# Kernel optimization log

Measured on AMD Instinct MI355X. Metric: run time of the kernel, lower is better.

Reference implementation:

```python
import jax, jax.numpy as jnp
import numpy as np

B, Hh, Ww, C = 8, 64, 64, 384
Dg = C // 2          # 192, per-group d_model
Di = Dg              # expand=1 -> d_inner = d_model
K = 2                # scan directions per group
S = 1                # d_state
R = -(-Dg // 16)     # dt_rank = ceil(d_model/16) = 12
Cout = 384


def setup_inputs() -> dict:
    key = jax.random.key(0)
    ks = jax.random.split(key, 30)
    n = lambda k, shp, s=0.05: (jax.random.normal(k, shp, jnp.float32) * s)
    inp = {
        "x": jax.random.normal(ks[0], (B, Hh * Ww, C), jnp.float32),
        "norm_g": jnp.ones((C,), jnp.float32),
        "norm_b": jnp.zeros((C,), jnp.float32),
        # DynamicChannelSorter (reduction=2)
        "r_w1": n(ks[1], (C // 2, C)), "r_b1": n(ks[2], (C // 2,)),
        "r_w2": n(ks[3], (C, C // 2)), "r_b2": n(ks[4], (C,)),
        # SS2D params stacked over 2 groups
        "in_proj_w": n(ks[5], (2, 2 * Di, Dg)),
        "conv_w": n(ks[6], (2, Di, 1, 3, 3), 0.1),
        "conv_b": n(ks[7], (2, Di), 0.02),
        "x_proj_w": n(ks[8], (2, K, R + 2 * S, Di)),
        "dt_proj_w": n(ks[9], (2, K, Di, R), 0.1),
        "dt_proj_b": n(ks[10], (2, K, Di), 0.5) - 3.0,   # softplus-inv of small dt
        "A_log": n(ks[11], (2, K, Di, S), 0.1),
        "Ds": jnp.ones((2, K, Di), jnp.float32),
        "out_norm_g": jnp.ones((2, Di), jnp.float32),
        "out_norm_b": jnp.zeros((2, Di), jnp.float32),
        "out_proj_w": n(ks[12], (2, Dg, Di)),
        # channel_interaction (reduction=16)
        "ci_w1": n(ks[13], (C // 16, C)), "ci_b1": n(ks[14], (C // 16,)),
        "ci_w2": n(ks[15], (C, C // 16)), "ci_b2": n(ks[16], (C,)),
        "proj_w": n(ks[17], (Cout, C)), "proj_b": n(ks[18], (Cout,)),
        "skip_scale": jnp.ones((1,), jnp.float32),
        "H": Hh, "W": Ww,
    }
    return inp


def _ln(x, g, b, eps=1e-5):
    m = x.mean(-1, keepdims=True)
    v = jnp.mean((x - m) ** 2, -1, keepdims=True)
    return (x - m) * jax.lax.rsqrt(v + eps) * g + b


def _selective_scan(xs, dts, Bm, Cm, A, D):
    # xs,dts: (B,K,Di,L); Bm,Cm: (B,K,S,L); A: (K,Di,S); D: (K,Di)
    dA = jnp.exp(dts[..., None] * A[None, :, :, None, :])              # (B,K,Di,L,S)
    dBx = dts[..., None] * jnp.swapaxes(Bm, -1, -2)[:, :, None] * xs[..., None]
    dA_t = jnp.moveaxis(dA, 3, 0)                                      # (L,B,K,Di,S)
    dBx_t = jnp.moveaxis(dBx, 3, 0)
    C_t = jnp.moveaxis(Cm, -1, 0)                                      # (L,B,K,S)
    h0 = jnp.zeros(dA.shape[:3] + (dA.shape[-1],), xs.dtype)           # (B,K,Di,S)

    def step(h, inp):
        a, bx, c = inp
        h = a * h + bx
        return h, jnp.einsum('bkcs,bks->bkc', h, c)

    _, ys = jax.lax.scan(step, h0, (dA_t, dBx_t, C_t))                 # (L,B,K,Di)
    ys = jnp.moveaxis(ys, 0, -1)                                       # (B,K,Di,L)
    return ys + D[None, :, :, None] * xs


def _ss2d(x, in_w, cw, cb, xp_w, dt_w, dt_b, A_log, D, on_g, on_b, op_w, vertical):
    # x: (B,H,W,Dg). VMamba-style SS2D with K=2 directions.
    b, h, w, _ = x.shape
    L = h * w
    xz = jnp.einsum('bhwc,dc->bhwd', x, in_w)                          # (B,H,W,2*Di)
    xc, z = jnp.split(xz, 2, axis=-1)
    xc = jnp.transpose(xc, (0, 3, 1, 2))                               # (B,Di,H,W)
    xc = jax.lax.conv_general_dilated(
        xc, cw, (1, 1), 'SAME', feature_group_count=Di,
        dimension_numbers=('NCHW', 'OIHW', 'NCHW')) + cb[None, :, None, None]
    xc = jax.nn.silu(xc)
    xf = jnp.transpose(xc, (0, 1, 3, 2)) if vertical else xc
    xflat = xf.reshape(b, Di, L)
    xs = jnp.stack([xflat, jnp.flip(xflat, -1)], axis=1)               # (B,K,Di,L)
    x_dbl = jnp.einsum('bkcl,kdc->bkdl', xs, xp_w)
    r = dt_w.shape[-1]
    dts, Bm, Cm = x_dbl[:, :, :r], x_dbl[:, :, r:r + S], x_dbl[:, :, r + S:r + 2 * S]
    dts = jax.nn.softplus(jnp.einsum('bkrl,kdr->bkdl', dts, dt_w) + dt_b[None, :, :, None])
    A = -jnp.exp(A_log)
    ys = _selective_scan(xs, dts, Bm, Cm, A, D)                        # (B,K,Di,L)
    y = ys[:, 0] + jnp.flip(ys[:, 1], -1)                              # cross-merge
    if vertical:
        y = jnp.transpose(y.reshape(b, Di, w, h), (0, 1, 3, 2))
    else:
        y = y.reshape(b, Di, h, w)
    y = jnp.transpose(y, (0, 2, 3, 1))                                 # (B,H,W,Di)
    y = _ln(y, on_g, on_b)
    y = y * jax.nn.silu(z)
    return jnp.einsum('bhwd,od->bhwo', y, op_w)


def reference(x, norm_g, norm_b, r_w1, r_b1, r_w2, r_b2, in_proj_w, conv_w,
              conv_b, x_proj_w, dt_proj_w, dt_proj_b, A_log, Ds, out_norm_g,
              out_norm_b, out_proj_w, ci_w1, ci_b1, ci_w2, ci_b2, proj_w,
              proj_b, skip_scale, H, W):
    b, n, c = x.shape
    residual = x
    xn = _ln(x, norm_g, norm_b)
    # dynamic channel sorter
    pool = xn.mean(axis=1)                                             # (B,C)
    scores = jax.nn.sigmoid(jax.nn.relu(pool @ r_w1.T + r_b1) @ r_w2.T + r_b2)
    sort_idx = jnp.argsort(-scores, axis=1)
    inv_idx = jnp.argsort(sort_idx, axis=1)
    x_sorted = jnp.take_along_axis(xn, sort_idx[:, None, :], axis=2)
    xsp = x_sorted.reshape(b, H, W, c)
    x1, x2 = jnp.split(xsp, 2, axis=-1)
    y1 = _ss2d(x1, in_proj_w[0], conv_w[0], conv_b[0], x_proj_w[0], dt_proj_w[0],
               dt_proj_b[0], A_log[0], Ds[0], out_norm_g[0], out_norm_b[0],
               out_proj_w[0], vertical=False)
    y2 = _ss2d(x2, in_proj_w[1], conv_w[1], conv_b[1], x_proj_w[1], dt_proj_w[1],
               dt_proj_b[1], A_log[1], Ds[1], out_norm_g[1], out_norm_b[1],
               out_proj_w[1], vertical=True)
    y_cat = jnp.concatenate([y1, y2], axis=-1).reshape(b, n, c)
    y_restored = jnp.take_along_axis(y_cat, inv_idx[:, None, :], axis=2)
    gate = jax.nn.sigmoid(jax.nn.relu(xn @ ci_w1.T + ci_b1) @ ci_w2.T + ci_b2)
    y_final = (y_restored * gate) @ proj_w.T + proj_b
    return residual + y_final * skip_scale
```

## Files before the change

kernel.cpp:

```cpp
#include <hip/hip_runtime.h>
#include <math.h>

#define NB 8
#define LTOK 4096
#define CH 384
#define DH 192
#define HH 64
#define WW 64
#define NCHK 128
#define CHS 32

static constexpr long BLC  = (long)NB * LTOK * CH;
static constexpr long CST  = (long)32 * NCHK * DH;

typedef unsigned short u16;
typedef u16   u16x8 __attribute__((ext_vector_type(8)));
typedef short s16x8 __attribute__((ext_vector_type(8)));
typedef float f32x4 __attribute__((ext_vector_type(4)));

__device__ inline u16 f2bf(float f){
  unsigned int u = __float_as_uint(f);
  return (u16)((u + 0x7FFFu + ((u >> 16) & 1u)) >> 16);
}
__device__ inline float bf2f(u16 h){ return __uint_as_float(((unsigned int)h) << 16); }
__device__ inline float fsigmoid(float x){ return 1.f / (1.f + __expf(-x)); }

#define SCOL(ml, c) ((c) ^ ((((ml) >> 2) & 3) << 4))

template<int NW>
__device__ inline float blockSum(float v, float* sm){
  #pragma unroll
  for (int o = 32; o > 0; o >>= 1) v += __shfl_down(v, o);
  int lane = threadIdx.x & 63, wv = threadIdx.x >> 6;
  if (lane == 0) sm[wv] = v;
  __syncthreads();
  if (threadIdx.x == 0){ float t = 0.f; for (int i = 0; i < NW; i++) t += sm[i]; sm[0] = t; }
  __syncthreads();
  float t = sm[0];
  __syncthreads();
  return t;
}

__global__ __launch_bounds__(128) void k_ln(const float* __restrict__ x,
    const float* __restrict__ g, const float* __restrict__ b, float* __restrict__ xn){
  __shared__ float sm[2];
  long row = blockIdx.x;
  int t = threadIdx.x;
  const float* xr = x + row * CH;
  float v0 = xr[t], v1 = xr[t + 128], v2 = xr[t + 256];
  float s = blockSum<2>(v0 + v1 + v2, sm);
  float m = s * (1.f / CH);
  float d0 = v0 - m, d1 = v1 - m, d2 = v2 - m;
  float vs = blockSum<2>(d0*d0 + d1*d1 + d2*d2, sm);
  float inv = rsqrtf(vs * (1.f / CH) + 1e-5f);
  float* o = xn + row * CH;
  o[t]       = d0 * inv * g[t]       + b[t];
  o[t + 128] = d1 * inv * g[t + 128] + b[t + 128];
  o[t + 256] = d2 * inv * g[t + 256] + b[t + 256];
}

__global__ __launch_bounds__(128) void k_pool(const float* __restrict__ xn, float* __restrict__ pp){
  int c = blockIdx.x * 128 + threadIdx.x;
  int chunk = blockIdx.y, b = blockIdx.z;
  long base = ((long)b * LTOK + chunk * 256) * CH;
  float s = 0.f;
  for (int n = 0; n < 256; n++) s += xn[base + (long)n * CH + c];
  pp[((long)b * 16 + chunk) * CH + c] = s;
}

__global__ __launch_bounds__(384) void k_score(const float* __restrict__ pp,
    const float* __restrict__ w1, const float* __restrict__ b1,
    const float* __restrict__ w2, const float* __restrict__ b2,
    int* __restrict__ sidx, int* __restrict__ inv){
  __shared__ float poolv[CH];
  __shared__ float hid[192];
  __shared__ float sc[CH];
  int b = blockIdx.x, t = threadIdx.x;
  float s = 0.f;
  for (int ch = 0; ch < 16; ch++) s += pp[((long)b * 16 + ch) * CH + t];
  poolv[t] = s * (1.f / LTOK);
  __syncthreads();
  if (t < 192){
    float h = b1[t];
    for (int c = 0; c < CH; c++) h += poolv[c] * w1[t * CH + c];
    hid[t] = fmaxf(h, 0.f);
  }
  __syncthreads();
  {
    float h = b2[t];
    for (int j = 0; j < 192; j++) h += hid[j] * w2[t * 192 + j];
    sc[t] = 1.f / (1.f + expf(-h));
  }
  __syncthreads();
  float mys = sc[t];
  int rank = 0;
  for (int j = 0; j < CH; j++){
    float o = sc[j];
    rank += (o > mys) || (o == mys && j < t);
  }
  sidx[b * CH + rank] = t;
  inv[b * CH + t] = rank;
}

__global__ __launch_bounds__(256) void k_cast(const float* __restrict__ s,
    u16* __restrict__ d, int n){
  int i = blockIdx.x * 256 + threadIdx.x;
  if (i < n) d[i] = f2bf(s[i]);
}

__global__ __launch_bounds__(256) void k_prepA(const float* __restrict__ alog,
    float* __restrict__ Atab){
  int i = blockIdx.x * 256 + threadIdx.x;
  if (i < 4 * 192) Atab[i] = -expf(alog[i]);
}

__global__ __launch_bounds__(256) void k_prepcw(const float* __restrict__ cw,
    u16* __restrict__ cwb){
  int i = blockIdx.x * 256 + threadIdx.x;
  if (i < 2 * 9 * DH){
    int g = i / (9 * DH); int r = i - g * 9 * DH;
    int tap = r / DH; int di = r - tap * DH;
    cwb[i] = f2bf(cw[((long)g * DH + di) * 9 + tap]);
  }
}

__global__ __launch_bounds__(384) void k_castgather(const float* __restrict__ xn,
    const int* __restrict__ sidx, u16* __restrict__ As){
  long row = blockIdx.x;
  int b = (int)(row >> 12);
  int t = threadIdx.x;
  int c = sidx[b * CH + t];
  As[row * CH + t] = f2bf(xn[row * CH + c]);
}

__global__ __launch_bounds__(256) void k_prepw(const float* __restrict__ w1,
    const float* __restrict__ b1, const float* __restrict__ w2,
    const int* __restrict__ sidx, u16* __restrict__ w1g, u16* __restrict__ w2p,
    float* __restrict__ b1p){
  int b = blockIdx.x, tid = threadIdx.x;
  if (b < NB){
    const int* sx = sidx + b * CH;
    for (int i = tid; i < 32 * CH; i += 256){
      int j = i / CH, r = i - j * CH;
      float v = (j < 24) ? w1[j * CH + sx[r]] : 0.f;
      w1g[(long)b * 32 * CH + i] = f2bf(v);
    }
  } else {
    for (int i = tid; i < CH * 32; i += 256){
      int n = i >> 5, j = i & 31;
      w2p[i] = f2bf((j < 24) ? w2[n * 24 + j] : 0.f);
    }
    if (tid < 32) b1p[tid] = (tid < 24) ? b1[tid] : 0.f;
  }
}

__global__ __launch_bounds__(256) void k_prepM(const float* __restrict__ dtw,
    const float* __restrict__ xpw, u16* __restrict__ Mw){
  int gk = blockIdx.y;
  int g = gk >> 1, k = gk & 1;
  int idx = blockIdx.x * 256 + threadIdx.x;
  int di = idx / 192, c = idx - di * 192;
  float s = 0.f;
  #pragma unroll
  for (int r = 0; r < 12; r++)
    s += dtw[((long)gk * 192 + di) * 12 + r] * xpw[(long)g * 5376 + (k * 14 + r) * 192 + c];
  Mw[(long)gk * 36864 + idx] = f2bf(s);
}

__global__ __launch_bounds__(256) void k_hid(const u16* __restrict__ As,
    const u16* __restrict__ w1g, const float* __restrict__ b1p,
    u16* __restrict__ hidp){
  __shared__ u16 sA[128 * 32];
  __shared__ u16 sB[32 * 32];
  int b = blockIdx.y;
  const u16* Ab = As + (long)b * LTOK * CH;
  const u16* Bb = w1g + (long)b * 32 * CH;
  int tid = threadIdx.x;
  int m0 = blockIdx.x * 128;
  int wv = tid >> 6, l = tid & 63;
  int wm = wv * 32;
  int kg = l >> 4, lr = l & 15;

  f32x4 acc[2][2];
  #pragma unroll
  for (int i = 0; i < 2; i++)
    #pragma unroll
    for (int j = 0; j < 2; j++)
      #pragma unroll
      for (int r = 0; r < 4; r++) acc[i][j][r] = 0.f;

  int aoffU[2], boffU[2];
  #pragma unroll
  for (int i = 0; i < 2; i++){
    int r = wm + i * 16 + lr;
    aoffU[i] = r * 32 + ((kg * 8) ^ ((r & 3) << 3));
  }
  #pragma unroll
  for (int j = 0; j < 2; j++){
    int r = j * 16 + lr;
    boffU[j] = r * 32 + ((kg * 8) ^ ((r & 3) << 3));
  }

  u16x8 ra[2], rbv;
  #pragma unroll
  for (int q = 0; q < 2; q++){
    int i = q * 256 + tid; int row = i >> 2, sl = i & 3, ss = sl ^ (row & 3);
    ra[q] = *(const u16x8*)(Ab + (long)(m0 + row) * CH + ss * 8);
  }
  if (tid < 128){
    int row = tid >> 2, sl = tid & 3, ss = sl ^ (row & 3);
    rbv = *(const u16x8*)(Bb + (long)row * CH + ss * 8);
  }

  const int nks = CH / 32;
  for (int ks = 0; ks < nks; ks++){
    __syncthreads();
    #pragma unroll
    for (int q = 0; q < 2; q++){
      int i = q * 256 + tid; int row = i >> 2, sl = i & 3;
      *(u16x8*)(sA + row * 32 + sl * 8) = ra[q];
    }
    if (tid < 128){
      int row = tid >> 2, sl = tid & 3;
      *(u16x8*)(sB + row * 32 + sl * 8) = rbv;
    }
    __syncthreads();
    if (ks + 1 < nks){
      int k0 = (ks + 1) * 32;
      #pragma unroll
      for (int q = 0; q < 2; q++){
        int i = q * 256 + tid; int row = i >> 2, sl = i & 3, ss = sl ^ (row & 3);
        ra[q] = *(const u16x8*)(Ab + (long)(m0 + row) * CH + k0 + ss * 8);
      }
      if (tid < 128){
        int row = tid >> 2, sl = tid & 3, ss = sl ^ (row & 3);
        rbv = *(const u16x8*)(Bb + (long)row * CH + k0 + ss * 8);
      }
    }
    s16x8 af[2], bfr[2];
    #pragma unroll
    for (int i = 0; i < 2; i++) af[i] = *(const s16x8*)(sA + aoffU[i]);
    #pragma unroll
    for (int j = 0; j < 2; j++) bfr[j] = *(const s16x8*)(sB + boffU[j]);
    #pragma unroll
    for (int i = 0; i < 2; i++)
      #pragma unroll
      for (int j = 0; j < 2; j++)
        acc[i][j] = __builtin_amdgcn_mfma_f32_16x16x32_bf16(af[i], bfr[j], acc[i][j], 0, 0, 0);
  }

  #pragma unroll
  for (int i = 0; i < 2; i++)
    #pragma unroll
    for (int j = 0; j < 2; j++)
      #pragma unroll
      for (int r = 0; r < 4; r++){
        int m = m0 + wm + i * 16 + kg * 4 + r;
        int n = j * 16 + lr;
        float v = fmaxf(acc[i][j][r] + b1p[n], 0.f);
        hidp[((long)b * LTOK + m) * 32 + n] = f2bf(v);
      }
}

template<int BN, int MODE>
__global__ __launch_bounds__(256) void k_mm(
    const u16* __restrict__ A, int lda, long aOuter, long aInner,
    const u16* __restrict__ B, long bInner,
    float* __restrict__ Cf, u16* __restrict__ Ch,
    long cOuter, long cInner, int ldc,
    int K, int innerCnt,
    const float* __restrict__ bias, const float* __restrict__ resid,
    const float* __restrict__ skip,
    const u16* __restrict__ gy, const int* __restrict__ ginv){
  constexpr int BM = 128;
  constexpr int AI = 2;
  constexpr int BI = (BN * 32) / (256 * 8);
  constexpr int NJ = BN / 32;
  __shared__ u16 sA[BM * 32];
  __shared__ u16 sB[BN * 32];

  int bz = blockIdx.z;
  int bo = bz / innerCnt, bi_ = bz - bo * innerCnt;
  const u16* Ab = A + (long)bo * aOuter + (long)bi_ * aInner;
  const u16* Bb = B + (long)bi_ * bInner;
  int tid = threadIdx.x;
  int m0 = blockIdx.y * BM, n0 = blockIdx.x * BN;
  int wv = tid >> 6, l = tid & 63;
  int wm = (wv >> 1) * 64, wn = (wv & 1) * (BN / 2);
  int kg = l >> 4, lr = l & 15;

  f32x4 acc[4][NJ];
  #pragma unroll
  for (int i = 0; i < 4; i++)
    #pragma unroll
    for (int j = 0; j < NJ; j++)
      #pragma unroll
      for (int r = 0; r < 4; r++) acc[i][j][r] = 0.f;

  int aoffU[4], boffU[NJ];
  #pragma unroll
  for (int i = 0; i < 4; i++){
    int r = wm + i * 16 + lr;
    aoffU[i] = r * 32 + ((kg * 8) ^ ((r & 3) << 3));
  }
  #pragma unroll
  for (int j = 0; j < NJ; j++){
    int r = wn + j * 16 + lr;
    boffU[j] = r * 32 + ((kg * 8) ^ ((r & 3) << 3));
  }

  u16x8 ra[AI], rb[BI];
  #pragma unroll
  for (int q = 0; q < AI; q++){
    int i = q * 256 + tid; int row = i >> 2, sl = i & 3, ss = sl ^ (row & 3);
    ra[q] = *(const u16x8*)(Ab + (long)(m0 + row) * lda + ss * 8);
  }
  #pragma unroll
  for (int q = 0; q < BI; q++){
    int i = q * 256 + tid; int row = i >> 2, sl = i & 3, ss = sl ^ (row & 3);
    rb[q] = *(const u16x8*)(Bb + (long)(n0 + row) * K + ss * 8);
  }

  int nks = K >> 5;
  for (int ks = 0; ks < nks; ks++){
    __syncthreads();
    #pragma unroll
    for (int q = 0; q < AI; q++){
      int i = q * 256 + tid; int row = i >> 2, sl = i & 3;
      *(u16x8*)(sA + row * 32 + sl * 8) = ra[q];
    }
    #pragma unroll
    for (int q = 0; q < BI; q++){
      int i = q * 256 + tid; int row = i >> 2, sl = i & 3;
      *(u16x8*)(sB + row * 32 + sl * 8) = rb[q];
    }
    __syncthreads();
    if (ks + 1 < nks){
      int k0 = (ks + 1) * 32;
      #pragma unroll
      for (int q = 0; q < AI; q++){
        int i = q * 256 + tid; int row = i >> 2, sl = i & 3, ss = sl ^ (row & 3);
        ra[q] = *(const u16x8*)(Ab + (long)(m0 + row) * lda + k0 + ss * 8);
      }
      #pragma unroll
      for (int q = 0; q < BI; q++){
        int i = q * 256 + tid; int row = i >> 2, sl = i & 3, ss = sl ^ (row & 3);
        rb[q] = *(const u16x8*)(Bb + (long)(n0 + row) * K + k0 + ss * 8);
      }
    }
    s16x8 af[4];
    #pragma unroll
    for (int i = 0; i < 4; i++) af[i] = *(const s16x8*)(sA + aoffU[i]);
    s16x8 bfr[NJ];
    #pragma unroll
    for (int j = 0; j < NJ; j++) bfr[j] = *(const s16x8*)(sB + boffU[j]);
    #pragma unroll
    for (int i = 0; i < 4; i++)
      #pragma unroll
      for (int j = 0; j < NJ; j++)
        acc[i][j] = __builtin_amdgcn_mfma_f32_16x16x32_bf16(af[i], bfr[j], acc[i][j], 0, 0, 0);
  }

  long zc = (long)bo * cOuter + (long)bi_ * cInner;
  #pragma unroll
  for (int i = 0; i < 4; i++){
    #pragma unroll
    for (int j = 0; j < NJ; j++){
      #pragma unroll
      for (int r = 0; r < 4; r++){
        int m = m0 + wm + i * 16 + kg * 4 + r;
        int n = n0 + wn + j * 16 + lr;
        float v = acc[i][j][r];
        if constexpr (MODE == 1){
          if (n < 192) ((u16*)Cf)[zc + (long)m * 192 + n] = f2bf(v);
          else         Ch[zc + (long)m * 192 + (n - 192)] = f2bf(v);
        } else if constexpr (MODE == 2){
          Ch[zc + (long)m * ldc + n] = f2bf(v);
        } else if constexpr (MODE == 3){
          float vb = v + bias[n];
          long o = (long)m * ldc + n;
          Cf[o] = resid[o] + skip[0] * vb;
        } else {
          float gate = fsigmoid(v + bias[n]);
          int bt = m >> 12;
          float yr = bf2f(gy[(long)m * ldc + ginv[bt * CH + n]]);
          Ch[(long)m * ldc + n] = f2bf(yr * gate);
        }
      }
    }
  }
}

__global__ __launch_bounds__(256) void k_dt(
    const u16* __restrict__ xcvh, const u16* __restrict__ Mw,
    const float* __restrict__ dtb, const float* __restrict__ Atab,
    const float* __restrict__ bc, u16* __restrict__ pk16,
    float* __restrict__ cP, float* __restrict__ cS){
  constexpr int BM = 128, AI = 2, NJ = 2;
  __shared__ unsigned sMem[BM * 64];
  u16* sA  = (u16*)sMem;
  u16* sB  = (u16*)(sMem + 2048);
  u16* xvT = (u16*)(sMem + 3072);

  int z = blockIdx.z;
  int bg = z >> 1, kk_ = z & 1, g = bg & 1, gk = g * 2 + kk_;
  const u16* Ab = xcvh + (long)bg * LTOK * 192;
  const u16* Bb = Mw + (long)gk * 36864;
  int tid = threadIdx.x;
  int m0 = blockIdx.y * BM, n0 = blockIdx.x * 64;
  int wv = tid >> 6, l = tid & 63;
  int wm = (wv >> 1) * 64, wn = (wv & 1) * 32;
  int kg = l >> 4, lr = l & 15;

  #pragma unroll
  for (int q = 0; q < 4; q++){
    int i8 = q * 256 + tid;
    int row = i8 >> 3, c8 = i8 & 7;
    u16x8 v = *(const u16x8*)(Ab + (long)(m0 + row) * 192 + n0 + c8 * 8);
    *(u16x8*)(xvT + row * 72 + c8 * 8) = v;
  }

  f32x4 acc[4][NJ];
  #pragma unroll
  for (int i = 0; i < 4; i++)
    #pragma unroll
    for (int j = 0; j < NJ; j++)
      #pragma unroll
      for (int r = 0; r < 4; r++) acc[i][j][r] = 0.f;

  int aoffU[4], boffU[NJ];
  #pragma unroll
  for (int i = 0; i < 4; i++){
    int r = wm + i * 16 + lr;
    aoffU[i] = r * 32 + ((kg * 8) ^ ((r & 3) << 3));
  }
  #pragma unroll
  for (int j = 0; j < NJ; j++){
    int r = wn + j * 16 + lr;
    boffU[j] = r * 32 + ((kg * 8) ^ ((r & 3) << 3));
  }

  u16x8 ra[AI], rb0;
  #pragma unroll
  for (int q = 0; q < AI; q++){
    int i = q * 256 + tid; int row = i >> 2, sl = i & 3, ss = sl ^ (row & 3);
    ra[q] = *(const u16x8*)(Ab + (long)(m0 + row) * 192 + ss * 8);
  }
  {
    int row = tid >> 2, sl = tid & 3, ss = sl ^ (row & 3);
    rb0 = *(const u16x8*)(Bb + (long)(n0 + row) * 192 + ss * 8);
  }

  const int nks = 6;
  for (int ks = 0; ks < nks; ks++){
    __syncthreads();
    #pragma unroll
    for (int q = 0; q < AI; q++){
      int i = q * 256 + tid; int row = i >> 2, sl = i & 3;
      *(u16x8*)(sA + row * 32 + sl * 8) = ra[q];
    }
    {
      int row = tid >> 2, sl = tid & 3;
      *(u16x8*)(sB + row * 32 + sl * 8) = rb0;
    }
    __syncthreads();
    if (ks + 1 < nks){
      int k0 = (ks + 1) * 32;
      #pragma unroll
      for (int q = 0; q < AI; q++){
        int i = q * 256 + tid; int row = i >> 2, sl = i & 3, ss = sl ^ (row & 3);
        ra[q] = *(const u16x8*)(Ab + (long)(m0 + row) * 192 + k0 + ss * 8);
      }
      {
        int row = tid >> 2, sl = tid & 3, ss = sl ^ (row & 3);
        rb0 = *(const u16x8*)(Bb + (long)(n0 + row) * 192 + k0 + ss * 8);
      }
    }
    s16x8 af[4], bfr[NJ];
    #pragma unroll
    for (int i = 0; i < 4; i++) af[i] = *(const s16x8*)(sA + aoffU[i]);
    #pragma unroll
    for (int j = 0; j < NJ; j++) bfr[j] = *(const s16x8*)(sB + boffU[j]);
    #pragma unroll
    for (int i = 0; i < 4; i++)
      #pragma unroll
      for (int j = 0; j < NJ; j++)
        acc[i][j] = __builtin_amdgcn_mfma_f32_16x16x32_bf16(af[i], bfr[j], acc[i][j], 0, 0, 0);
  }

  unsigned pkreg[4][NJ][4];
  float dtbj[NJ], Atlj[NJ];
  #pragma unroll
  for (int j = 0; j < NJ; j++){
    int n = n0 + wn + j * 16 + lr;
    dtbj[j] = dtb[gk * 192 + n];
    Atlj[j] = Atab[gk * 192 + n];
  }
  #pragma unroll
  for (int i = 0; i < 4; i++){
    #pragma unroll
    for (int r = 0; r < 4; r++){
      int ml = wm + i * 16 + kg * 4 + r;
      int m = m0 + ml;
      float Bv = bc[((long)z * LTOK + m) * 2];
      #pragma unroll
      for (int j = 0; j < NJ; j++){
        int n = n0 + wn + j * 16 + lr;
        float rr = acc[i][j][r] + dtbj[j];
        float dtv = __logf(1.f + __expf(rr));
        float av  = __expf(Atlj[j] * dtv);
        float xv  = bf2f(xvT[ml * 72 + wn + j * 16 + lr]);
        pk16[((long)z * LTOK + m) * 192 + n] = f2bf(dtv);
        pkreg[i][j][r] = ((unsigned)f2bf(dtv * Bv * xv) << 16) | (unsigned)f2bf(av);
      }
    }
  }

  __syncthreads();
  #pragma unroll
  for (int i = 0; i < 4; i++){
    #pragma unroll
    for (int j = 0; j < NJ; j++){
      #pragma unroll
      for (int r = 0; r < 4; r++){
        int ml = wm + i * 16 + kg * 4 + r;
        int cl = wn + j * 16 + lr;
        sMem[ml * 64 + SCOL(ml, cl)] = pkreg[i][j][r];
      }
    }
  }
  __syncthreads();

  int cc = tid >> 6, nn = tid & 63;
  float P = 1.f, S = 0.f;
  if (kk_ == 0){
    for (int s = 0; s < CHS; s++){
      int row = cc * CHS + s;
      unsigned v = sMem[row * 64 + SCOL(row, nn)];
      float a = bf2f((u16)(v & 0xFFFFu));
      float dBx = bf2f((u16)(v >> 16));
      P *= a; S = a * S + dBx;
    }
  } else {
    for (int s = CHS - 1; s >= 0; s--){
      int row = cc * CHS + s;
      unsigned v = sMem[row * 64 + SCOL(row, nn)];
      float a = bf2f((u16)(v & 0xFFFFu));
      float dBx = bf2f((u16)(v >> 16));
      P *= a; S = a * S + dBx;
    }
  }
  int cglob = (kk_ == 0) ? (blockIdx.y * 4 + cc)
                         : ((LTOK - m0) / CHS - cc - 1);
  long idx = ((long)z * NCHK + cglob) * 192 + n0 + nn;
  cP[idx] = P;
  cS[idx] = S;
}

__global__ __launch_bounds__(192) void k_conv(const u16* __restrict__ xch,
    const u16* __restrict__ cwb, const float* __restrict__ cb,
    const float* __restrict__ xpw, u16* __restrict__ xcvh,
    float* __restrict__ bc){
  __shared__ float red[8][4][25];
  int tid = threadIdx.x;
  int chg = tid % 24, pp = tid / 24;
  int p = blockIdx.x * 8 + pp;
  int bg = blockIdx.y; int g = bg & 1;
  int h = p >> 6, w = p & 63;
  int di = chg * 8;
  long sb = (long)bg * LTOK;

  u16x8 wv[9];
  #pragma unroll
  for (int t = 0; t < 9; t++)
    wv[t] = *(const u16x8*)(cwb + ((long)g * 9 + t) * DH + di);

  float acc[8];
  #pragma unroll
  for (int j = 0; j < 8; j++) acc[j] = cb[g * DH + di + j];

  #pragma unroll
  for (int dh = -1; dh <= 1; dh++){
    int hh = h + dh; if (hh < 0 || hh >= HH) continue;
    #pragma unroll
    for (int dw = -1; dw <= 1; dw++){
      int ww2 = w + dw; if (ww2 < 0 || ww2 >= WW) continue;
      u16x8 xv = *(const u16x8*)(xch + (sb + hh * WW + ww2) * DH + di);
      int t = (dh + 1) * 3 + (dw + 1);
      #pragma unroll
      for (int j = 0; j < 8; j++) acc[j] += bf2f(wv[t][j]) * bf2f(xv[j]);
    }
  }

  u16x8 ov;
  #pragma unroll
  for (int j = 0; j < 8; j++){
    float s = acc[j];
    acc[j] = s * fsigmoid(s);
    ov[j] = f2bf(acc[j]);
  }
  int lscan = (g == 0) ? p : (w * HH + h);
  *(u16x8*)(xcvh + (sb + lscan) * DH + di) = ov;

  #pragma unroll
  for (int j = 0; j < 4; j++){
    int k = j >> 1, ci = j & 1;
    const float* wl = xpw + (long)g * 5376 + (k * 14 + 12 + ci) * 192 + di;
    float sacc = 0.f;
    #pragma unroll
    for (int q = 0; q < 8; q++) sacc += acc[q] * wl[q];
    red[pp][j][chg] = sacc;
  }
  __syncthreads();
  if (tid < 32){
    int pos = tid >> 2, j = tid & 3;
    float ssum = 0.f;
    #pragma unroll
    for (int q = 0; q < 24; q++) ssum += red[pos][j][q];
    int p2 = blockIdx.x * 8 + pos;
    int h2 = p2 >> 6, w2 = p2 & 63;
    int ls = (g == 0) ? p2 : (w2 * HH + h2);
    int k = j >> 1;
    bc[(((long)(bg * 2 + k)) * LTOK + ls) * 2 + (j & 1)] = ssum;
  }
}

__global__ __launch_bounds__(192) void k_scan_p2(const float* __restrict__ cP,
    const float* __restrict__ cS, float* __restrict__ h0){
  int z = blockIdx.x;
  int di = threadIdx.x;
  float h = 0.f;
  for (int c = 0; c < NCHK; c++){
    long idx = ((long)z * NCHK + c) * 192 + di;
    h0[idx] = h;
    h = cP[idx] * h + cS[idx];
  }
}

__global__ __launch_bounds__(192) void k_scan_p3(const u16* __restrict__ pk16,
    const u16* __restrict__ xcvh, const float* __restrict__ bc,
    const float* __restrict__ Atab, const float* __restrict__ ds,
    const float* __restrict__ h0, const u16* __restrict__ zh,
    const float* __restrict__ ong, const float* __restrict__ onb,
    u16* __restrict__ yab){
  __shared__ float yl[CHS][193];
  __shared__ float red[2][32][6];
  __shared__ float minv[2][32];
  int bg = blockIdx.x, c = blockIdx.y;
  int g = bg & 1;
  int di = threadIdx.x;
  const u16* xc = xcvh + (long)bg * LTOK * 192 + di;
  int l0 = c * CHS;
  float yv[CHS];

  {
    int z = bg * 2, gk = g * 2;
    float Dv = ds[gk * 192 + di], Av = Atab[gk * 192 + di];
    const u16* pk = pk16 + (long)z * LTOK * 192 + di;
    const float* bcp = bc + (long)z * LTOK * 2;
    float h = h0[((long)z * NCHK + c) * 192 + di];
    #pragma unroll
    for (int s = 0; s < CHS; s++){
      int l = l0 + s;
      float dtv = bf2f(pk[(long)l * 192]);
      float av  = __expf(Av * dtv);
      float xv  = bf2f(xc[(long)l * 192]);
      float Bv  = bcp[l * 2], Cv = bcp[l * 2 + 1];
      h = av * h + dtv * Bv * xv;
      yv[s] = h * Cv + Dv * xv;
    }
  }
  {
    int z = bg * 2 + 1, gk = g * 2 + 1;
    float Dv = ds[gk * 192 + di], Av = Atab[gk * 192 + di];
    const u16* pk = pk16 + (long)z * LTOK * 192 + di;
    const float* bcp = bc + (long)z * LTOK * 2;
    int cc = NCHK - 1 - c;
    float h = h0[((long)z * NCHK + cc) * 192 + di];
    #pragma unroll
    for (int s = CHS - 1; s >= 0; s--){
      int l = l0 + s;
      float dtv = bf2f(pk[(long)l * 192]);
      float av  = __expf(Av * dtv);
      float xv  = bf2f(xc[(long)l * 192]);
      float Bv  = bcp[l * 2], Cv = bcp[l * 2 + 1];
      h = av * h + dtv * Bv * xv;
      yv[s] += h * Cv + Dv * xv;
    }
  }

  #pragma unroll
  for (int s = 0; s < CHS; s++) yl[s][di] = yv[s];
  __syncthreads();
  {
    int pos = di & 31, seg = di >> 5;
    float s1 = 0.f, s2 = 0.f;
    #pragma unroll
    for (int q = 0; q < 32; q++){
      float v = yl[pos][seg * 32 + q];
      s1 += v; s2 += v * v;
    }
    red[0][pos][seg] = s1;
    red[1][pos][seg] = s2;
  }
  __syncthreads();
  if (di < 32){
    float s1 = 0.f, s2 = 0.f;
    #pragma unroll
    for (int q = 0; q < 6; q++){ s1 += red[0][di][q]; s2 += red[1][di][q]; }
    float m = s1 * (1.f / DH);
    float var = s2 * (1.f / DH) - m * m;
    minv[0][di] = m;
    minv[1][di] = rsqrtf(var + 1e-5f);
  }
  __syncthreads();

  float gng = ong[g * 192 + di], gnb = onb[g * 192 + di];
  long zbase = (long)bg * LTOK;
  #pragma unroll
  for (int s = 0; s < CHS; s++){
    int l = l0 + s;
    int p = (g == 0) ? l : ((l & 63) * 64 + (l >> 6));
    float m = minv[0][s], inv = minv[1][s];
    float yln = (yv[s] - m) * inv * gng + gnb;
    float z = bf2f(zh[(zbase + p) * 192 + di]);
    yab[(zbase + p) * 192 + di] = f2bf(yln * z * fsigmoid(z));
  }
}

extern "C" void kernel_launch(void* const* d_in, const int* in_sizes, int n_in,
                              void* d_out, int out_size, void* d_ws, size_t ws_size,
                              hipStream_t stream){
  const float* x       = (const float*)d_in[0];
  const float* norm_g  = (const float*)d_in[1];
  const float* norm_b  = (const float*)d_in[2];
  const float* r_w1    = (const float*)d_in[3];
  const float* r_b1    = (const float*)d_in[4];
  const float* r_w2    = (const float*)d_in[5];
  const float* r_b2    = (const float*)d_in[6];
  const float* in_proj = (const float*)d_in[7];
  const float* conv_w  = (const float*)d_in[8];
  const float* conv_b  = (const float*)d_in[9];
  const float* xp_w    = (const float*)d_in[10];
  const float* dt_w    = (const float*)d_in[11];
  const float* dt_b    = (const float*)d_in[12];
  const float* A_log   = (const float*)d_in[13];
  const float* Ds      = (const float*)d_in[14];
  const float* on_g    = (const float*)d_in[15];
  const float* on_b    = (const float*)d_in[16];
  const float* op_w    = (const float*)d_in[17];
  const float* ci_w1   = (const float*)d_in[18];
  const float* ci_b1   = (const float*)d_in[19];
  const float* ci_w2   = (const float*)d_in[20];
  const float* ci_b2   = (const float*)d_in[21];
  const float* proj_w  = (const float*)d_in[22];
  const float* proj_b  = (const float*)d_in[23];
  const float* skip    = (const float*)d_in[24];
  float* out = (float*)d_out;
  float* ws  = (float*)d_ws;

  float* xn   = ws;
  float* xcb  = ws + BLC;
  float* R3   = ws + 2 * BLC;
  float* R4   = R3 + BLC / 2;
  float* R5   = R4 + BLC / 2;
  float* pp   = R5 + BLC / 2;
  int*  sidx  = (int*)(pp + NB * 16 * CH);
  int*  inv   = sidx + NB * CH;
  u16*  wip   = (u16*)(inv + NB * CH);
  u16*  wop   = wip + 2 * 384 * 192;
  u16*  wpj   = wop + 2 * 192 * 192;
  u16*  w1g   = wpj + 384 * 384;
  u16*  w2p   = w1g + NB * 32 * CH;
  u16*  Mw    = w2p + CH * 32;
  u16*  cwb   = Mw + 4 * 192 * 192;
  float* b1p  = (float*)(cwb + 2 * 9 * DH);
  float* Atab = b1p + 32;
  u16*  hidp  = (u16*)(Atab + 4 * 192);
  float* bc   = (float*)(hidp + (long)NB * LTOK * 32);
  float* cP   = bc + 32 * LTOK * 2;
  float* cS   = cP + CST;
  float* h0   = cS + CST;

  size_t need = ((size_t)(2 * BLC) + 3 * (BLC / 2) + NB * 16 * CH + 32 * LTOK * 2 + 3 * CST + 64) * 4
              + (size_t)(2 * NB * CH) * 4 + (size_t)(4 * 192 + 32) * 4
              + ((size_t)2*384*192 + 2*192*192 + 384*384 + NB*32*CH + CH*32 + 4*192*192
                 + 2*9*DH + (size_t)NB * LTOK * 32) * 2
              + 8192;
  if (ws_size < need) return;

  u16*  As   = (u16*)R5;
  u16*  zh   = (u16*)R3;
  u16*  xcbh = (u16*)xcb;
  u16*  xcvh = (u16*)R4;
  u16*  pk16 = (u16*)ws;
  u16*  yab  = (u16*)R5;
  u16*  ycat = (u16*)R3;
  u16*  gab  = (u16*)xcb;

  k_ln<<<NB * LTOK, 128, 0, stream>>>(x, norm_g, norm_b, xn);
  k_cast<<<(2*384*192 + 255)/256, 256, 0, stream>>>(in_proj, wip, 2*384*192);
  k_cast<<<(2*192*192 + 255)/256, 256, 0, stream>>>(op_w,    wop, 2*192*192);
  k_cast<<<(384*384   + 255)/256, 256, 0, stream>>>(proj_w,  wpj, 384*384);
  k_prepA<<<3, 256, 0, stream>>>(A_log, Atab);
  k_prepcw<<<(2*9*DH + 255)/256, 256, 0, stream>>>(conv_w, cwb);
  k_prepM<<<dim3(144, 4), 256, 0, stream>>>(dt_w, xp_w, Mw);
  k_pool<<<dim3(3, 16, NB), 128, 0, stream>>>(xn, pp);
  k_score<<<NB, 384, 0, stream>>>(pp, r_w1, r_b1, r_w2, r_b2, sidx, inv);
  k_castgather<<<NB * LTOK, 384, 0, stream>>>(xn, sidx, As);
  k_prepw<<<NB + 1, 256, 0, stream>>>(ci_w1, ci_b1, ci_w2, sidx, w1g, w2p, b1p);

  k_mm<128, 1><<<dim3(3, 32, 16), 256, 0, stream>>>(
      As, CH, (long)LTOK * CH, 192,
      wip, (long)384 * 192,
      (float*)xcbh, zh, (long)2 * LTOK * DH, (long)LTOK * DH, 0,
      192, 2, nullptr, nullptr, nullptr, nullptr, nullptr);

  k_hid<<<dim3(32, NB), 256, 0, stream>>>(As, w1g, b1p, hidp);

  k_conv<<<dim3(LTOK / 8, NB * 2), 192, 0, stream>>>(xcbh, cwb, conv_b, xp_w, xcvh, bc);

  k_dt<<<dim3(3, 32, 32), 256, 0, stream>>>(xcvh, Mw, dt_b, Atab, bc, pk16, cP, cS);

  k_scan_p2<<<32, 192, 0, stream>>>(cP, cS, h0);

  k_scan_p3<<<dim3(NB * 2, NCHK), 192, 0, stream>>>(
      pk16, xcvh, bc, Atab, Ds, h0, zh, on_g, on_b, yab);

  k_mm<64, 2><<<dim3(3, 32, 16), 256, 0, stream>>>(
      yab, DH, (long)2 * LTOK * DH, (long)LTOK * DH,
      wop, (long)192 * 192,
      nullptr, ycat, (long)LTOK * CH, 192, CH,
      192, 2, nullptr, nullptr, nullptr, nullptr, nullptr);

  k_mm<128, 4><<<dim3(3, 256, 1), 256, 0, stream>>>(
      hidp, 32, 0, 0,
      w2p, 0,
      nullptr, gab, 0, 0, CH,
      32, 1, ci_b2, nullptr, nullptr, ycat, inv);

  k_mm<128, 3><<<dim3(3, 256, 1), 256, 0, stream>>>(
      gab, CH, 0, 0,
      wpj, 0,
      out, nullptr, 0, 0, CH,
      CH, 1, proj_b, x, skip, nullptr, nullptr);
}
```

Baseline: 369.8 us.

## Shrink k_dt tile to 64 rows and precompute SiLU(z) in in_proj epilogue

The k_dt kernel drops from 128-row to 64-row tiles, which doubles the grid and halves LDS use. It also drops the staged xvT copy and reads x values straight from global memory, and only two waves do the chunk scan. Separately, the SiLU on the z gate moves from the scan_p3 epilogue into the in_proj GEMM epilogue, so scan_p3 does a single multiply. The aim is better occupancy and load balance for k_dt, and less sigmoid work in the scan. The cost is more redundant B-weight loads, idle waves in the scan phase, and uncoalesced global reads for xv.

```diff
diff --git a/kernel.cpp b/kernel.cpp
--- a/kernel.cpp
+++ b/kernel.cpp
@@ -373,7 +373,7 @@
         float v = acc[i][j][r];
         if constexpr (MODE == 1){
           if (n < 192) ((u16*)Cf)[zc + (long)m * 192 + n] = f2bf(v);
-          else         Ch[zc + (long)m * 192 + (n - 192)] = f2bf(v);
+          else         Ch[zc + (long)m * 192 + (n - 192)] = f2bf(v * fsigmoid(v));
         } else if constexpr (MODE == 2){
           Ch[zc + (long)m * ldc + n] = f2bf(v);
         } else if constexpr (MODE == 3){
@@ -396,41 +396,32 @@
     const float* __restrict__ dtb, const float* __restrict__ Atab,
     const float* __restrict__ bc, u16* __restrict__ pk16,
     float* __restrict__ cP, float* __restrict__ cS){
-  constexpr int BM = 128, AI = 2, NJ = 2;
-  __shared__ unsigned sMem[BM * 64];
-  u16* sA  = (u16*)sMem;
-  u16* sB  = (u16*)(sMem + 2048);
-  u16* xvT = (u16*)(sMem + 3072);
+  constexpr int NJ = 2;
+  __shared__ unsigned sMem[64 * 64];
+  u16* sA = (u16*)sMem;
+  u16* sB = (u16*)(sMem + 1024);
 
   int z = blockIdx.z;
   int bg = z >> 1, kk_ = z & 1, g = bg & 1, gk = g * 2 + kk_;
   const u16* Ab = xcvh + (long)bg * LTOK * 192;
   const u16* Bb = Mw + (long)gk * 36864;
   int tid = threadIdx.x;
-  int m0 = blockIdx.y * BM, n0 = blockIdx.x * 64;
+  int m0 = blockIdx.y * 64, n0 = blockIdx.x * 64;
   int wv = tid >> 6, l = tid & 63;
-  int wm = (wv >> 1) * 64, wn = (wv & 1) * 32;
+  int wm = (wv >> 1) * 32, wn = (wv & 1) * 32;
   int kg = l >> 4, lr = l & 15;
 
-  #pragma unroll
-  for (int q = 0; q < 4; q++){
-    int i8 = q * 256 + tid;
-    int row = i8 >> 3, c8 = i8 & 7;
-    u16x8 v = *(const u16x8*)(Ab + (long)(m0 + row) * 192 + n0 + c8 * 8);
-    *(u16x8*)(xvT + row * 72 + c8 * 8) = v;
-  }
-
-  f32x4 acc[4][NJ];
-  #pragma unroll
-  for (int i = 0; i < 4; i++)
+  f32x4 acc[2][NJ];
+  #pragma unroll
+  for (int i = 0; i < 2; i++)
     #pragma unroll
     for (int j = 0; j < NJ; j++)
       #pragma unroll
       for (int r = 0; r < 4; r++) acc[i][j][r] = 0.f;
 
-  int aoffU[4], boffU[NJ];
-  #pragma unroll
-  for (int i = 0; i < 4; i++){
+  int aoffU[2], boffU[NJ];
+  #pragma unroll
+  for (int i = 0; i < 2; i++){
     int r = wm + i * 16 + lr;
     aoffU[i] = r * 32 + ((kg * 8) ^ ((r & 3) << 3));
   }
@@ -440,55 +431,35 @@
     boffU[j] = r * 32 + ((kg * 8) ^ ((r & 3) << 3));
   }
 
-  u16x8 ra[AI], rb0;
-  #pragma unroll
-  for (int q = 0; q < AI; q++){
-    int i = q * 256 + tid; int row = i >> 2, sl = i & 3, ss = sl ^ (row & 3);
-    ra[q] = *(const u16x8*)(Ab + (long)(m0 + row) * 192 + ss * 8);
-  }
-  {
-    int row = tid >> 2, sl = tid & 3, ss = sl ^ (row & 3);
-    rb0 = *(const u16x8*)(Bb + (long)(n0 + row) * 192 + ss * 8);
-  }
+  int srow = tid >> 2, ssl = tid & 3, sss = ssl ^ (srow & 3);
+  u16x8 ra, rb0;
+  ra  = *(const u16x8*)(Ab + (long)(m0 + srow) * 192 + sss * 8);
+  rb0 = *(const u16x8*)(Bb + (long)(n0 + srow) * 192 + sss * 8);
 
   const int nks = 6;
   for (int ks = 0; ks < nks; ks++){
     __syncthreads();
-    #pragma unroll
-    for (int q = 0; q < AI; q++){
-      int i = q * 256 + tid; int row = i >> 2, sl = i & 3;
-      *(u16x8*)(sA + row * 32 + sl * 8) = ra[q];
-    }
-    {
-      int row = tid >> 2, sl = tid & 3;
-      *(u16x8*)(sB + row * 32 + sl * 8) = rb0;
-    }
+    *(u16x8*)(sA + srow * 32 + ssl * 8) = ra;
+    *(u16x8*)(sB + srow * 32 + ssl * 8) = rb0;
     __syncthreads();
     if (ks + 1 < nks){
       int k0 = (ks + 1) * 32;
-      #pragma unroll
-      for (int q = 0; q < AI; q++){
-        int i = q * 256 + tid; int row = i >> 2, sl = i & 3, ss = sl ^ (row & 3);
-        ra[q] = *(const u16x8*)(Ab + (long)(m0 + row) * 192 + k0 + ss * 8);
-      }
-      {
-        int row = tid >> 2, sl = tid & 3, ss = sl ^ (row & 3);
-        rb0 = *(const u16x8*)(Bb + (long)(n0 + row) * 192 + k0 + ss * 8);
-      }
-    }
-    s16x8 af[4], bfr[NJ];
-    #pragma unroll
-    for (int i = 0; i < 4; i++) af[i] = *(const s16x8*)(sA + aoffU[i]);
+      ra  = *(const u16x8*)(Ab + (long)(m0 + srow) * 192 + k0 + sss * 8);
+      rb0 = *(const u16x8*)(Bb + (long)(n0 + srow) * 192 + k0 + sss * 8);
+    }
+    s16x8 af[2], bfr[NJ];
+    #pragma unroll
+    for (int i = 0; i < 2; i++) af[i] = *(const s16x8*)(sA + aoffU[i]);
     #pragma unroll
     for (int j = 0; j < NJ; j++) bfr[j] = *(const s16x8*)(sB + boffU[j]);
     #pragma unroll
-    for (int i = 0; i < 4; i++)
+    for (int i = 0; i < 2; i++)
       #pragma unroll
       for (int j = 0; j < NJ; j++)
         acc[i][j] = __builtin_amdgcn_mfma_f32_16x16x32_bf16(af[i], bfr[j], acc[i][j], 0, 0, 0);
   }
 
-  unsigned pkreg[4][NJ][4];
+  unsigned pkreg[2][NJ][4];
   float dtbj[NJ], Atlj[NJ];
   #pragma unroll
   for (int j = 0; j < NJ; j++){
@@ -497,7 +468,7 @@
     Atlj[j] = Atab[gk * 192 + n];
   }
   #pragma unroll
-  for (int i = 0; i < 4; i++){
+  for (int i = 0; i < 2; i++){
     #pragma unroll
     for (int r = 0; r < 4; r++){
       int ml = wm + i * 16 + kg * 4 + r;
@@ -509,7 +480,7 @@
         float rr = acc[i][j][r] + dtbj[j];
         float dtv = __logf(1.f + __expf(rr));
         float av  = __expf(Atlj[j] * dtv);
-        float xv  = bf2f(xvT[ml * 72 + wn + j * 16 + lr]);
+        float xv  = bf2f(xcvh[((long)bg * LTOK + m) * 192 + n]);
         pk16[((long)z * LTOK + m) * 192 + n] = f2bf(dtv);
         pkreg[i][j][r] = ((unsigned)f2bf(dtv * Bv * xv) << 16) | (unsigned)f2bf(av);
       }
@@ -518,7 +489,7 @@
 
   __syncthreads();
   #pragma unroll
-  for (int i = 0; i < 4; i++){
+  for (int i = 0; i < 2; i++){
     #pragma unroll
     for (int j = 0; j < NJ; j++){
       #pragma unroll
@@ -531,30 +502,32 @@
   }
   __syncthreads();
 
-  int cc = tid >> 6, nn = tid & 63;
-  float P = 1.f, S = 0.f;
-  if (kk_ == 0){
-    for (int s = 0; s < CHS; s++){
-      int row = cc * CHS + s;
-      unsigned v = sMem[row * 64 + SCOL(row, nn)];
-      float a = bf2f((u16)(v & 0xFFFFu));
-      float dBx = bf2f((u16)(v >> 16));
-      P *= a; S = a * S + dBx;
-    }
-  } else {
-    for (int s = CHS - 1; s >= 0; s--){
-      int row = cc * CHS + s;
-      unsigned v = sMem[row * 64 + SCOL(row, nn)];
-      float a = bf2f((u16)(v & 0xFFFFu));
-      float dBx = bf2f((u16)(v >> 16));
-      P *= a; S = a * S + dBx;
-    }
-  }
-  int cglob = (kk_ == 0) ? (blockIdx.y * 4 + cc)
-                         : ((LTOK - m0) / CHS - cc - 1);
-  long idx = ((long)z * NCHK + cglob) * 192 + n0 + nn;
-  cP[idx] = P;
-  cS[idx] = S;
+  if (tid < 128){
+    int cc = tid >> 6, nn = tid & 63;
+    float P = 1.f, S = 0.f;
+    if (kk_ == 0){
+      for (int s = 0; s < CHS; s++){
+        int row = cc * CHS + s;
+        unsigned v = sMem[row * 64 + SCOL(row, nn)];
+        float a = bf2f((u16)(v & 0xFFFFu));
+        float dBx = bf2f((u16)(v >> 16));
+        P *= a; S = a * S + dBx;
+      }
+    } else {
+      for (int s = CHS - 1; s >= 0; s--){
+        int row = cc * CHS + s;
+        unsigned v = sMem[row * 64 + SCOL(row, nn)];
+        float a = bf2f((u16)(v & 0xFFFFu));
+        float dBx = bf2f((u16)(v >> 16));
+        P *= a; S = a * S + dBx;
+      }
+    }
+    int cglob = (kk_ == 0) ? (blockIdx.y * 2 + cc)
+                           : (NCHK - 1 - blockIdx.y * 2 - cc);
+    long idx = ((long)z * NCHK + cglob) * 192 + n0 + nn;
+    cP[idx] = P;
+    cS[idx] = S;
+  }
 }
 
 __global__ __launch_bounds__(192) void k_conv(const u16* __restrict__ xch,
@@ -640,7 +613,7 @@
 __global__ __launch_bounds__(192) void k_scan_p3(const u16* __restrict__ pk16,
     const u16* __restrict__ xcvh, const float* __restrict__ bc,
     const float* __restrict__ Atab, const float* __restrict__ ds,
-    const float* __restrict__ h0, const u16* __restrict__ zh,
+    const float* __restrict__ h0, const u16* __restrict__ zsh,
     const float* __restrict__ ong, const float* __restrict__ onb,
     u16* __restrict__ yab){
   __shared__ float yl[CHS][193];
@@ -723,8 +696,8 @@
     int p = (g == 0) ? l : ((l & 63) * 64 + (l >> 6));
     float m = minv[0][s], inv = minv[1][s];
     float yln = (yv[s] - m) * inv * gng + gnb;
-    float z = bf2f(zh[(zbase + p) * 192 + di]);
-    yab[(zbase + p) * 192 + di] = f2bf(yln * z * fsigmoid(z));
+    float zs = bf2f(zsh[(zbase + p) * 192 + di]);
+    yab[(zbase + p) * 192 + di] = f2bf(yln * zs);
   }
 }
 
@@ -790,7 +763,7 @@
   if (ws_size < need) return;
 
   u16*  As   = (u16*)R5;
-  u16*  zh   = (u16*)R3;
+  u16*  zsh  = (u16*)R3;
   u16*  xcbh = (u16*)xcb;
   u16*  xcvh = (u16*)R4;
   u16*  pk16 = (u16*)ws;
@@ -813,19 +786,19 @@
   k_mm<128, 1><<<dim3(3, 32, 16), 256, 0, stream>>>(
       As, CH, (long)LTOK * CH, 192,
       wip, (long)384 * 192,
-      (float*)xcbh, zh, (long)2 * LTOK * DH, (long)LTOK * DH, 0,
+      (float*)xcbh, zsh, (long)2 * LTOK * DH, (long)LTOK * DH, 0,
       192, 2, nullptr, nullptr, nullptr, nullptr, nullptr);
 
   k_hid<<<dim3(32, NB), 256, 0, stream>>>(As, w1g, b1p, hidp);
 
   k_conv<<<dim3(LTOK / 8, NB * 2), 192, 0, stream>>>(xcbh, cwb, conv_b, xp_w, xcvh, bc);
 
-  k_dt<<<dim3(3, 32, 32), 256, 0, stream>>>(xcvh, Mw, dt_b, Atab, bc, pk16, cP, cS);
+  k_dt<<<dim3(3, 64, 32), 256, 0, stream>>>(xcvh, Mw, dt_b, Atab, bc, pk16, cP, cS);
 
   k_scan_p2<<<32, 192, 0, stream>>>(cP, cS, h0);
 
   k_scan_p3<<<dim3(NB * 2, NCHK), 192, 0, stream>>>(
-      pk16, xcvh, bc, Atab, Ds, h0, zh, on_g, on_b, yab);
+      pk16, xcvh, bc, Atab, Ds, h0, zsh, on_g, on_b, yab);
 
   k_mm<64, 2><<<dim3(3, 32, 16), 256, 0, stream>>>(
       yab, DH, (long)2 * LTOK * DH, (long)LTOK * DH,
```

Result: faster. 357.2 us (-3.4%).
